# Kernel optimization log

Measured on AMD Instinct MI355X. Metric: run time of the kernel, lower is better.

## Reference

```python
import jax, jax.numpy as jnp
import numpy as np

T, H, E, I, IS = 1024, 2048, 64, 512, 1024
TOP_K = 8
CAP = 256


def setup_inputs() -> dict:
    key = jax.random.key(0)
    ks = jax.random.split(key, 9)
    s = 0.02
    return {
        "hidden_states": jax.random.normal(ks[0], (T, H), jnp.float32),
        "gate_w": jax.random.normal(ks[1], (E, H), jnp.float32) * s,
        "w1": jax.random.normal(ks[2], (E, H, I), jnp.float32) * s,
        "w3": jax.random.normal(ks[3], (E, H, I), jnp.float32) * s,
        "w2": jax.random.normal(ks[4], (E, I, H), jnp.float32) * s,
        "ws1": jax.random.normal(ks[5], (H, IS), jnp.float32) * s,
        "ws3": jax.random.normal(ks[6], (H, IS), jnp.float32) * s,
        "ws2": jax.random.normal(ks[7], (IS, H), jnp.float32) * s,
        "wsg": jax.random.normal(ks[8], (H, 1), jnp.float32) * s,
    }


def reference(hidden_states, gate_w, w1, w3, w2, ws1, ws3, ws2, wsg):
    x = hidden_states  # [T, H]
    n_tok = x.shape[0]

    # ---- router (Renormalize: top-k over logits, softmax over selected) ----
    logits = x @ gate_w.T                                  # [T, E]
    top_vals, top_idx = jax.lax.top_k(logits, TOP_K)       # [T, k]
    route_w = jax.nn.softmax(top_vals, axis=-1)            # renormalized weights

    # ---- dispatch: flatten (token, slot) assignments, rank within expert ----
    e = top_idx.reshape(-1)                                # [T*k] expert ids
    t = jnp.repeat(jnp.arange(n_tok), TOP_K)               # [T*k] token ids
    w_flat = route_w.reshape(-1)
    order = jnp.argsort(e, stable=True)
    counts = jax.ops.segment_sum(jnp.ones_like(e), e, num_segments=E)
    starts = jnp.cumsum(counts) - counts                   # exclusive cumsum
    pos_sorted = jnp.arange(e.shape[0]) - starts[e[order]]
    pos = jnp.zeros_like(e).at[order].set(pos_sorted)      # rank within expert
    valid = pos < CAP
    slot = jnp.where(valid, e * CAP + pos, E * CAP)        # overflow -> dump slot

    buf = jnp.zeros((E * CAP + 1, x.shape[1]), x.dtype).at[slot].set(x[t])
    xb = buf[:-1].reshape(E, CAP, x.shape[1])              # [E, C, H]

    # ---- grouped SwiGLU experts ----
    g = jax.nn.silu(jnp.einsum('ech,ehi->eci', xb, w1))
    u = jnp.einsum('ech,ehi->eci', xb, w3)
    yb = jnp.einsum('eci,eih->ech', g * u, w2).reshape(E * CAP, -1)

    # ---- combine ----
    contrib = yb[jnp.minimum(slot, E * CAP - 1)] * (w_flat * valid)[:, None]
    routed = jnp.zeros_like(x).at[t].add(contrib)

    # ---- shared expert with sigmoid gate ----
    shared = (jax.nn.silu(x @ ws1) * (x @ ws3)) @ ws2
    shared = jax.nn.sigmoid(x @ wsg) * shared

    return routed + shared
```

## Files before the change

### kernel.cpp

```cpp
#include <hip/hip_runtime.h>
#include <hip/hip_bf16.h>

#define NT    1024
#define HDIM  2048
#define NEXP  64
#define IDIM  512
#define ISDIM 1024
#define KTOP  8
#define ECAP  256

typedef float  f32x4 __attribute__((ext_vector_type(4)));
typedef __bf16 bf16x8 __attribute__((ext_vector_type(8)));
typedef unsigned short u16x8 __attribute__((ext_vector_type(8)));

static __device__ __forceinline__ unsigned short f2b(float f) {
  __hip_bfloat16 h = __float2bfloat16(f);
  return __builtin_bit_cast(unsigned short, h);
}
static __device__ __forceinline__ float b2f(unsigned short u) {
  return __bfloat162float(__builtin_bit_cast(__hip_bfloat16, u));
}
static __device__ __forceinline__ void sync_lds() {
  __builtin_amdgcn_s_waitcnt(0xc07f);
  __builtin_amdgcn_s_barrier();
}

__global__ __launch_bounds__(256) void k_router(
    const float* __restrict__ x, const float* __restrict__ gw,
    const float* __restrict__ wsg,
    int* __restrict__ counts, int* __restrict__ tok_list,
    int* __restrict__ slot_map, float* __restrict__ wgt_map,
    float* __restrict__ gate_sig)
{
  __shared__ float xs[HDIM];
  __shared__ float lg[NEXP];
  __shared__ float selv[KTOP];
  __shared__ int   sele[KTOP];
  const int t = blockIdx.x, tid = threadIdx.x;
  const float* xr = x + (size_t)t * HDIM;
  for (int i = tid; i < HDIM / 4; i += 256)
    ((f32x4*)xs)[i] = ((const f32x4*)xr)[i];
  __syncthreads();
  const int wave = tid >> 6, lane = tid & 63;
  for (int ei = 0; ei < 16; ++ei) {
    const int e = wave * 16 + ei;
    const float* g = gw + (size_t)e * HDIM;
    float s = 0.f;
    for (int j = lane; j < HDIM; j += 64) s += xs[j] * g[j];
    for (int off = 32; off; off >>= 1) s += __shfl_xor(s, off, 64);
    if (lane == 0) lg[e] = s;
  }
  if (wave == 1) {
    float s = 0.f;
    for (int j = lane; j < HDIM; j += 64) s += xs[j] * wsg[j];
    for (int off = 32; off; off >>= 1) s += __shfl_xor(s, off, 64);
    if (lane == 0) gate_sig[t] = 1.f / (1.f + __expf(-s));
  }
  __syncthreads();
  if (wave == 0) {
    float v = lg[lane];
    for (int k = 0; k < KTOP; ++k) {
      float m = v;
      for (int off = 32; off; off >>= 1) m = fmaxf(m, __shfl_xor(m, off, 64));
      unsigned long long msk = __ballot(v == m);
      int src = __ffsll(msk) - 1;
      if (lane == src) v = -3.4e38f;
      if (lane == 0) { selv[k] = m; sele[k] = src; }
    }
  }
  __syncthreads();
  if (tid < KTOP) {
    const int k = tid;
    const float mx = selv[0];
    float sum = 0.f;
    for (int i = 0; i < KTOP; ++i) sum += __expf(selv[i] - mx);
    const float w = __expf(selv[k] - mx) / sum;
    const int e = sele[k];
    const int pos = atomicAdd(&counts[e], 1);
    int slot = -1;
    if (pos < ECAP) { slot = e * ECAP + pos; tok_list[slot] = t; }
    slot_map[t * KTOP + k] = slot;
    wgt_map[t * KTOP + k] = w;
  }
}

__global__ __launch_bounds__(512, 2) void k_gemm1(
    const float* __restrict__ x,
    const float* __restrict__ w1, const float* __restrict__ w3,
    const float* __restrict__ ws1, const float* __restrict__ ws3,
    const int* __restrict__ counts, const int* __restrict__ tok_list,
    unsigned short* __restrict__ hbuf, unsigned short* __restrict__ hsbuf)
{
  __shared__ unsigned short lds[32768];
  const int g = blockIdx.y, ntile = blockIdx.x, tid = threadIdx.x;
  const bool is_exp = (g < NEXP);
  int me, ldb, m0s = 0;
  const float *b1p, *b3p;
  const int n0 = ntile * 128;
  if (is_exp) {
    if (ntile >= IDIM / 128) return;
    me = counts[g]; me = me < ECAP ? me : ECAP;
    if (me == 0) return;
    ldb = IDIM;
    b1p = w1 + (size_t)g * HDIM * IDIM + n0;
    b3p = w3 + (size_t)g * HDIM * IDIM + n0;
  } else {
    me = 256; ldb = ISDIM;
    m0s = (g - NEXP) * 256;
    b1p = ws1 + n0;
    b3p = ws3 + n0;
  }
  const int ar = tid >> 1, kh = (tid & 1) * 16;
  bool avalid;
  const float* arow;
  if (is_exp) {
    avalid = (ar < me);
    const int tok = avalid ? tok_list[g * ECAP + ar] : 0;
    arow = x + (size_t)tok * HDIM + kh;
  } else {
    avalid = true;
    arow = x + (size_t)(m0s + ar) * HDIM + kh;
  }
  const int ag0 = kh >> 3;
  const int aoff0 = ar * 32 + (((ag0 + 0) ^ (ar & 3)) << 3);
  const int aoff1 = ar * 32 + (((ag0 + 1) ^ (ar & 3)) << 3);
  const int bkr = tid >> 4, bc8 = (tid & 15) * 8;
  const float* b1t = b1p + (size_t)bkr * ldb + bc8;
  const float* b3t = b3p + (size_t)bkr * ldb + bc8;
  int boff[8];
#pragma unroll
  for (int i = 0; i < 8; ++i) {
    const int n = bc8 + i;
    boff[i] = n * 32 + (((bkr >> 3) ^ (n & 3)) << 3) + (bkr & 7);
  }
  const int lane = tid & 63, quad = lane >> 4, l15 = lane & 15;
  const int wv = tid >> 6, wm = wv >> 1, wn = wv & 1;
  const bool wactive = (wm * 64 < me);
  int aro[4], bo[4];
#pragma unroll
  for (int i = 0; i < 4; ++i) {
    const int rr = wm * 64 + i * 16 + l15;
    aro[i] = rr * 32 + ((quad ^ (rr & 3)) << 3);
    const int nn = wn * 64 + i * 16 + l15;
    bo[i] = nn * 32 + ((quad ^ (nn & 3)) << 3);
  }
  f32x4 acc1[4][4], acc3[4][4];
#pragma unroll
  for (int i = 0; i < 4; ++i)
#pragma unroll
    for (int j = 0; j < 4; ++j) {
      acc1[i][j] = f32x4{0.f, 0.f, 0.f, 0.f};
      acc3[i][j] = f32x4{0.f, 0.f, 0.f, 0.f};
    }
  f32x4 arg[4], b1r[2], b3r[2];
  const int KT = HDIM / 32;
  if (avalid) {
    arg[0] = ((const f32x4*)arow)[0]; arg[1] = ((const f32x4*)arow)[1];
    arg[2] = ((const f32x4*)arow)[2]; arg[3] = ((const f32x4*)arow)[3];
  }
  b1r[0] = ((const f32x4*)b1t)[0]; b1r[1] = ((const f32x4*)b1t)[1];
  b3r[0] = ((const f32x4*)b3t)[0]; b3r[1] = ((const f32x4*)b3t)[1];

  for (int kt = 0; kt < KT; ++kt) {
    unsigned short* L = lds + (kt & 1) * 16384;
    if (avalid) {
      u16x8 p0, p1;
#pragma unroll
      for (int i = 0; i < 4; ++i) {
        p0[i] = f2b(arg[0][i]); p0[4 + i] = f2b(arg[1][i]);
        p1[i] = f2b(arg[2][i]); p1[4 + i] = f2b(arg[3][i]);
      }
      *(u16x8*)&L[aoff0] = p0;
      *(u16x8*)&L[aoff1] = p1;
    }
    {
      unsigned short* B1 = L + 8192;
      unsigned short* B3 = L + 12288;
#pragma unroll
      for (int i = 0; i < 4; ++i) { B1[boff[i]] = f2b(b1r[0][i]); B1[boff[4 + i]] = f2b(b1r[1][i]); }
#pragma unroll
      for (int i = 0; i < 4; ++i) { B3[boff[i]] = f2b(b3r[0][i]); B3[boff[4 + i]] = f2b(b3r[1][i]); }
    }
    if (kt + 1 < KT) {
      const float* ap = arow + (kt + 1) * 32;
      if (avalid) {
        arg[0] = ((const f32x4*)ap)[0]; arg[1] = ((const f32x4*)ap)[1];
        arg[2] = ((const f32x4*)ap)[2]; arg[3] = ((const f32x4*)ap)[3];
      }
      const float* bp1 = b1t + (size_t)(kt + 1) * 32 * ldb;
      b1r[0] = ((const f32x4*)bp1)[0]; b1r[1] = ((const f32x4*)bp1)[1];
      const float* bp3 = b3t + (size_t)(kt + 1) * 32 * ldb;
      b3r[0] = ((const f32x4*)bp3)[0]; b3r[1] = ((const f32x4*)bp3)[1];
    }
    sync_lds();
    if (wactive) {
      bf16x8 af[4], bf1[4], bf3[4];
#pragma unroll
      for (int i = 0; i < 4; ++i)
        af[i] = __builtin_bit_cast(bf16x8, *(const u16x8*)&L[aro[i]]);
#pragma unroll
      for (int j = 0; j < 4; ++j) {
        bf1[j] = __builtin_bit_cast(bf16x8, *(const u16x8*)&L[8192 + bo[j]]);
        bf3[j] = __builtin_bit_cast(bf16x8, *(const u16x8*)&L[12288 + bo[j]]);
      }
#pragma unroll
      for (int i = 0; i < 4; ++i)
#pragma unroll
        for (int j = 0; j < 4; ++j) {
          acc1[i][j] = __builtin_amdgcn_mfma_f32_16x16x32_bf16(af[i], bf1[j], acc1[i][j], 0, 0, 0);
          acc3[i][j] = __builtin_amdgcn_mfma_f32_16x16x32_bf16(af[i], bf3[j], acc3[i][j], 0, 0, 0);
        }
    }
  }
  if (wactive) {
#pragma unroll
    for (int i = 0; i < 4; ++i) {
#pragma unroll
      for (int q = 0; q < 4; ++q) {
        const int rr = wm * 64 + i * 16 + quad * 4 + q;
        if (is_exp && rr >= me) continue;
        unsigned short* orow = is_exp
            ? hbuf + ((size_t)g * ECAP + rr) * IDIM
            : hsbuf + (size_t)(m0s + rr) * ISDIM;
#pragma unroll
        for (int j = 0; j < 4; ++j) {
          const int col = n0 + wn * 64 + j * 16 + l15;
          const float gg = acc1[i][j][q];
          const float uu = acc3[i][j][q];
          const float sv = (gg / (1.f + __expf(-gg))) * uu;
          orow[col] = f2b(sv);
        }
      }
    }
  }
}

__global__ __launch_bounds__(512, 2) void k_gemm2(
    const unsigned short* __restrict__ hbuf, const unsigned short* __restrict__ hsbuf,
    const float* __restrict__ w2, const float* __restrict__ ws2,
    const int* __restrict__ counts, const float* __restrict__ gate_sig,
    unsigned short* __restrict__ yb, float* __restrict__ out)
{
  __shared__ unsigned short lds[24576];
  const int g = blockIdx.y, ntile = blockIdx.x, tid = threadIdx.x;
  const bool is_exp = (g < NEXP);
  int me, K, m0s = 0;
  const unsigned short* abase;
  const float* bbase;
  const int n0 = ntile * 128;
  if (is_exp) {
    me = counts[g]; me = me < ECAP ? me : ECAP;
    if (me == 0) return;
    K = IDIM;
    abase = hbuf + (size_t)g * ECAP * IDIM;
    bbase = w2 + (size_t)g * IDIM * HDIM + n0;
  } else {
    me = 256; K = ISDIM;
    m0s = (g - NEXP) * 256;
    abase = hsbuf + (size_t)m0s * ISDIM;
    bbase = ws2 + n0;
  }
  const int ar = tid >> 1, kh = (tid & 1) * 16;
  const bool avalid = (ar < me);
  const unsigned short* arow = abase + (size_t)ar * K + kh;
  const int ag0 = kh >> 3;
  const int aoff0 = ar * 32 + (((ag0 + 0) ^ (ar & 3)) << 3);
  const int aoff1 = ar * 32 + (((ag0 + 1) ^ (ar & 3)) << 3);
  const int bkr = tid >> 4, bc8 = (tid & 15) * 8;
  const float* bt = bbase + (size_t)bkr * HDIM + bc8;
  int boff[8];
#pragma unroll
  for (int i = 0; i < 8; ++i) {
    const int n = bc8 + i;
    boff[i] = n * 32 + (((bkr >> 3) ^ (n & 3)) << 3) + (bkr & 7);
  }
  const int lane = tid & 63, quad = lane >> 4, l15 = lane & 15;
  const int wv = tid >> 6, wm = wv >> 1, wn = wv & 1;
  const bool wactive = (wm * 64 < me);
  int aro[4], bo[4];
#pragma unroll
  for (int i = 0; i < 4; ++i) {
    const int rr = wm * 64 + i * 16 + l15;
    aro[i] = rr * 32 + ((quad ^ (rr & 3)) << 3);
    const int nn = wn * 64 + i * 16 + l15;
    bo[i] = nn * 32 + ((quad ^ (nn & 3)) << 3);
  }
  f32x4 acc[4][4];
#pragma unroll
  for (int i = 0; i < 4; ++i)
#pragma unroll
    for (int j = 0; j < 4; ++j) acc[i][j] = f32x4{0.f, 0.f, 0.f, 0.f};
  u16x8 a0r, a1r;
  f32x4 br[2];
  const int KT = K / 32;
  if (avalid) { a0r = ((const u16x8*)arow)[0]; a1r = ((const u16x8*)arow)[1]; }
  br[0] = ((const f32x4*)bt)[0]; br[1] = ((const f32x4*)bt)[1];

  for (int kt = 0; kt < KT; ++kt) {
    unsigned short* L = lds + (kt & 1) * 12288;
    if (avalid) { *(u16x8*)&L[aoff0] = a0r; *(u16x8*)&L[aoff1] = a1r; }
    {
      unsigned short* B = L + 8192;
#pragma unroll
      for (int i = 0; i < 4; ++i) { B[boff[i]] = f2b(br[0][i]); B[boff[4 + i]] = f2b(br[1][i]); }
    }
    if (kt + 1 < KT) {
      const unsigned short* ap = arow + (kt + 1) * 32;
      if (avalid) { a0r = ((const u16x8*)ap)[0]; a1r = ((const u16x8*)ap)[1]; }
      const float* bp = bt + (size_t)(kt + 1) * 32 * HDIM;
      br[0] = ((const f32x4*)bp)[0]; br[1] = ((const f32x4*)bp)[1];
    }
    sync_lds();
    if (wactive) {
      bf16x8 af[4], bfr[4];
#pragma unroll
      for (int i = 0; i < 4; ++i)
        af[i] = __builtin_bit_cast(bf16x8, *(const u16x8*)&L[aro[i]]);
#pragma unroll
      for (int j = 0; j < 4; ++j)
        bfr[j] = __builtin_bit_cast(bf16x8, *(const u16x8*)&L[8192 + bo[j]]);
#pragma unroll
      for (int i = 0; i < 4; ++i)
#pragma unroll
        for (int j = 0; j < 4; ++j)
          acc[i][j] = __builtin_amdgcn_mfma_f32_16x16x32_bf16(af[i], bfr[j], acc[i][j], 0, 0, 0);
    }
  }
  if (wactive) {
#pragma unroll
    for (int i = 0; i < 4; ++i) {
#pragma unroll
      for (int q = 0; q < 4; ++q) {
        const int rr = wm * 64 + i * 16 + quad * 4 + q;
        if (is_exp) {
          if (rr >= me) continue;
          unsigned short* orow = yb + ((size_t)g * ECAP + rr) * HDIM;
#pragma unroll
          for (int j = 0; j < 4; ++j) {
            const int col = n0 + wn * 64 + j * 16 + l15;
            orow[col] = f2b(acc[i][j][q]);
          }
        } else {
          const float gt = gate_sig[m0s + rr];
          float* orow = out + (size_t)(m0s + rr) * HDIM;
#pragma unroll
          for (int j = 0; j < 4; ++j) {
            const int col = n0 + wn * 64 + j * 16 + l15;
            orow[col] = gt * acc[i][j][q];
          }
        }
      }
    }
  }
}

__global__ __launch_bounds__(256) void k_combine(
    const unsigned short* __restrict__ yb,
    const int* __restrict__ slot_map, const float* __restrict__ wgt_map,
    float* __restrict__ out)
{
  __shared__ int ss[KTOP];
  __shared__ float ww[KTOP];
  const int t = blockIdx.x, tid = threadIdx.x;
  if (tid < KTOP) { ss[tid] = slot_map[t * KTOP + tid]; ww[tid] = wgt_map[t * KTOP + tid]; }
  __syncthreads();
  const int c = tid * 8;
  float* op = out + (size_t)t * HDIM + c;
  f32x4 o0 = ((const f32x4*)op)[0];
  f32x4 o1 = ((const f32x4*)op)[1];
  for (int k = 0; k < KTOP; ++k) {
    const int s = ss[k];
    if (s < 0) continue;
    const float w = ww[k];
    const u16x8 y = *(const u16x8*)(yb + (size_t)s * HDIM + c);
#pragma unroll
    for (int i = 0; i < 4; ++i) {
      o0[i] += w * b2f(y[i]);
      o1[i] += w * b2f(y[4 + i]);
    }
  }
  ((f32x4*)op)[0] = o0;
  ((f32x4*)op)[1] = o1;
}

extern "C" void kernel_launch(void* const* d_in, const int* in_sizes, int n_in,
                              void* d_out, int out_size, void* d_ws, size_t ws_size,
                              hipStream_t stream) {
  (void)in_sizes; (void)n_in; (void)out_size; (void)ws_size;
  const float* x   = (const float*)d_in[0];
  const float* gw  = (const float*)d_in[1];
  const float* w1  = (const float*)d_in[2];
  const float* w3  = (const float*)d_in[3];
  const float* w2  = (const float*)d_in[4];
  const float* ws1 = (const float*)d_in[5];
  const float* ws3 = (const float*)d_in[6];
  const float* ws2 = (const float*)d_in[7];
  const float* wsg = (const float*)d_in[8];
  float* out = (float*)d_out;
  char* ws = (char*)d_ws;
  int*   counts   = (int*)ws;
  int*   tok_list = (int*)(ws + 256);
  int*   slot_map = (int*)(ws + 256 + (64 << 10));
  float* wgt_map  = (float*)(ws + 256 + (96 << 10));
  float* gate_sig = (float*)(ws + 256 + (128 << 10));
  unsigned short* hbuf  = (unsigned short*)(ws + (1 << 20));
  unsigned short* hsbuf = (unsigned short*)(ws + (17 << 20));
  unsigned short* yb    = (unsigned short*)(ws + (19 << 20));

  hipMemsetAsync(counts, 0, 256, stream);
  k_router<<<dim3(NT), dim3(256), 0, stream>>>(x, gw, wsg, counts, tok_list,
                                               slot_map, wgt_map, gate_sig);
  k_gemm1<<<dim3(8, NEXP + 4), dim3(512), 0, stream>>>(x, w1, w3, ws1, ws3,
                                                       counts, tok_list, hbuf, hsbuf);
  k_gemm2<<<dim3(16, NEXP + 4), dim3(512), 0, stream>>>(hbuf, hsbuf, w2, ws2,
                                                        counts, gate_sig, yb, out);
  k_combine<<<dim3(NT), dim3(256), 0, stream>>>(yb, slot_map, wgt_map, out);
}
```

Before: 1.250 ms.

## Flatten GEMM grids with XCD-aware block remap and vectorized B-tile LDS stores

Both grouped GEMM kernels now launch a flat 1D grid with no idle blocks and remap block IDs so consecutive logical tiles land on the same XCD (the remap assumes 8 chiplets), aiming for better L2 reuse of weights and expert inputs. The B-operand staging changes from row-vector loads with eight scalar LDS stores to column-wise scalar global loads (coalesced across threads) packed into one 16-byte LDS store per matrix. The LDS swizzle gains an extra XOR term to reduce bank conflicts. The trade-off is eight strided scalar global loads per thread per k-step instead of two vector loads.

New measurement: 1.099 ms. -12.0%, faster.

```diff
diff --git a/kernel.cpp b/kernel.cpp
--- a/kernel.cpp
+++ b/kernel.cpp
@@ -12,6 +12,8 @@
 typedef float  f32x4 __attribute__((ext_vector_type(4)));
 typedef __bf16 bf16x8 __attribute__((ext_vector_type(8)));
 typedef unsigned short u16x8 __attribute__((ext_vector_type(8)));
+
+#define SWZ(r, q) ((((q) ^ ((r) & 3) ^ (((r) >> 2) & 3)) & 3) << 3)
 
 static __device__ __forceinline__ unsigned short f2b(float f) {
   __hip_bfloat16 h = __float2bfloat16(f);
@@ -92,25 +94,33 @@
     unsigned short* __restrict__ hbuf, unsigned short* __restrict__ hsbuf)
 {
   __shared__ unsigned short lds[32768];
-  const int g = blockIdx.y, ntile = blockIdx.x, tid = threadIdx.x;
-  const bool is_exp = (g < NEXP);
-  int me, ldb, m0s = 0;
+  const int cpx = gridDim.x >> 3;
+  const int b0 = blockIdx.x;
+  const int bid = (b0 & 7) * cpx + (b0 >> 3);
+  const int tid = threadIdx.x;
+  bool is_exp;
+  int g, ntile, me, ldb, m0s = 0;
   const float *b1p, *b3p;
-  const int n0 = ntile * 128;
-  if (is_exp) {
-    if (ntile >= IDIM / 128) return;
+  if (bid < NEXP * 4) {
+    is_exp = true; g = bid >> 2; ntile = bid & 3;
     me = counts[g]; me = me < ECAP ? me : ECAP;
     if (me == 0) return;
     ldb = IDIM;
+  } else {
+    is_exp = false;
+    const int s = bid - NEXP * 4;
+    g = s >> 3; ntile = s & 7;
+    me = 256; ldb = ISDIM; m0s = g * 256;
+  }
+  const int n0 = ntile * 128;
+  if (is_exp) {
     b1p = w1 + (size_t)g * HDIM * IDIM + n0;
     b3p = w3 + (size_t)g * HDIM * IDIM + n0;
   } else {
-    me = 256; ldb = ISDIM;
-    m0s = (g - NEXP) * 256;
     b1p = ws1 + n0;
     b3p = ws3 + n0;
   }
-  const int ar = tid >> 1, kh = (tid & 1) * 16;
+  const int ar = tid & 255, sel = tid >> 8, kh = sel * 16;
   bool avalid;
   const float* arow;
   if (is_exp) {
@@ -121,18 +131,12 @@
     avalid = true;
     arow = x + (size_t)(m0s + ar) * HDIM + kh;
   }
-  const int ag0 = kh >> 3;
-  const int aoff0 = ar * 32 + (((ag0 + 0) ^ (ar & 3)) << 3);
-  const int aoff1 = ar * 32 + (((ag0 + 1) ^ (ar & 3)) << 3);
-  const int bkr = tid >> 4, bc8 = (tid & 15) * 8;
-  const float* b1t = b1p + (size_t)bkr * ldb + bc8;
-  const float* b3t = b3p + (size_t)bkr * ldb + bc8;
-  int boff[8];
-#pragma unroll
-  for (int i = 0; i < 8; ++i) {
-    const int n = bc8 + i;
-    boff[i] = n * 32 + (((bkr >> 3) ^ (n & 3)) << 3) + (bkr & 7);
-  }
+  const int aoff0 = ar * 32 + SWZ(ar, sel * 2);
+  const int aoff1 = ar * 32 + SWZ(ar, sel * 2 + 1);
+  const int bn = tid & 127, bg = tid >> 7;
+  const float* b1c = b1p + (size_t)(bg * 8) * ldb + bn;
+  const float* b3c = b3p + (size_t)(bg * 8) * ldb + bn;
+  const int boffB = bn * 32 + SWZ(bn, bg);
   const int lane = tid & 63, quad = lane >> 4, l15 = lane & 15;
   const int wv = tid >> 6, wm = wv >> 1, wn = wv & 1;
   const bool wactive = (wm * 64 < me);
@@ -140,9 +144,9 @@
 #pragma unroll
   for (int i = 0; i < 4; ++i) {
     const int rr = wm * 64 + i * 16 + l15;
-    aro[i] = rr * 32 + ((quad ^ (rr & 3)) << 3);
+    aro[i] = rr * 32 + SWZ(rr, quad);
     const int nn = wn * 64 + i * 16 + l15;
-    bo[i] = nn * 32 + ((quad ^ (nn & 3)) << 3);
+    bo[i] = nn * 32 + SWZ(nn, quad);
   }
   f32x4 acc1[4][4], acc3[4][4];
 #pragma unroll
@@ -152,14 +156,18 @@
       acc1[i][j] = f32x4{0.f, 0.f, 0.f, 0.f};
       acc3[i][j] = f32x4{0.f, 0.f, 0.f, 0.f};
     }
-  f32x4 arg[4], b1r[2], b3r[2];
+  f32x4 arg[4];
+  float b1v[8], b3v[8];
   const int KT = HDIM / 32;
   if (avalid) {
     arg[0] = ((const f32x4*)arow)[0]; arg[1] = ((const f32x4*)arow)[1];
     arg[2] = ((const f32x4*)arow)[2]; arg[3] = ((const f32x4*)arow)[3];
   }
-  b1r[0] = ((const f32x4*)b1t)[0]; b1r[1] = ((const f32x4*)b1t)[1];
-  b3r[0] = ((const f32x4*)b3t)[0]; b3r[1] = ((const f32x4*)b3t)[1];
+#pragma unroll
+  for (int j = 0; j < 8; ++j) {
+    b1v[j] = b1c[(size_t)j * ldb];
+    b3v[j] = b3c[(size_t)j * ldb];
+  }
 
   for (int kt = 0; kt < KT; ++kt) {
     unsigned short* L = lds + (kt & 1) * 16384;
@@ -174,12 +182,11 @@
       *(u16x8*)&L[aoff1] = p1;
     }
     {
-      unsigned short* B1 = L + 8192;
-      unsigned short* B3 = L + 12288;
-#pragma unroll
-      for (int i = 0; i < 4; ++i) { B1[boff[i]] = f2b(b1r[0][i]); B1[boff[4 + i]] = f2b(b1r[1][i]); }
-#pragma unroll
-      for (int i = 0; i < 4; ++i) { B3[boff[i]] = f2b(b3r[0][i]); B3[boff[4 + i]] = f2b(b3r[1][i]); }
+      u16x8 pb1, pb3;
+#pragma unroll
+      for (int j = 0; j < 8; ++j) { pb1[j] = f2b(b1v[j]); pb3[j] = f2b(b3v[j]); }
+      *(u16x8*)&L[8192 + boffB] = pb1;
+      *(u16x8*)&L[12288 + boffB] = pb3;
     }
     if (kt + 1 < KT) {
       const float* ap = arow + (kt + 1) * 32;
@@ -187,10 +194,13 @@
         arg[0] = ((const f32x4*)ap)[0]; arg[1] = ((const f32x4*)ap)[1];
         arg[2] = ((const f32x4*)ap)[2]; arg[3] = ((const f32x4*)ap)[3];
       }
-      const float* bp1 = b1t + (size_t)(kt + 1) * 32 * ldb;
-      b1r[0] = ((const f32x4*)bp1)[0]; b1r[1] = ((const f32x4*)bp1)[1];
-      const float* bp3 = b3t + (size_t)(kt + 1) * 32 * ldb;
-      b3r[0] = ((const f32x4*)bp3)[0]; b3r[1] = ((const f32x4*)bp3)[1];
+      const float* p1 = b1c + (size_t)(kt + 1) * 32 * ldb;
+      const float* p3 = b3c + (size_t)(kt + 1) * 32 * ldb;
+#pragma unroll
+      for (int j = 0; j < 8; ++j) {
+        b1v[j] = p1[(size_t)j * ldb];
+        b3v[j] = p3[(size_t)j * ldb];
+      }
     }
     sync_lds();
     if (wactive) {
@@ -242,38 +252,37 @@
     unsigned short* __restrict__ yb, float* __restrict__ out)
 {
   __shared__ unsigned short lds[24576];
-  const int g = blockIdx.y, ntile = blockIdx.x, tid = threadIdx.x;
-  const bool is_exp = (g < NEXP);
-  int me, K, m0s = 0;
+  const int cpx = gridDim.x >> 3;
+  const int b0 = blockIdx.x;
+  const int bid = (b0 & 7) * cpx + (b0 >> 3);
+  const int tid = threadIdx.x;
+  bool is_exp;
+  int g, ntile, me, K, m0s = 0;
   const unsigned short* abase;
   const float* bbase;
-  const int n0 = ntile * 128;
-  if (is_exp) {
+  if (bid < NEXP * 16) {
+    is_exp = true; g = bid >> 4; ntile = bid & 15;
     me = counts[g]; me = me < ECAP ? me : ECAP;
     if (me == 0) return;
     K = IDIM;
     abase = hbuf + (size_t)g * ECAP * IDIM;
-    bbase = w2 + (size_t)g * IDIM * HDIM + n0;
   } else {
-    me = 256; K = ISDIM;
-    m0s = (g - NEXP) * 256;
+    is_exp = false;
+    const int s = bid - NEXP * 16;
+    g = s >> 4; ntile = s & 15;
+    me = 256; K = ISDIM; m0s = g * 256;
     abase = hsbuf + (size_t)m0s * ISDIM;
-    bbase = ws2 + n0;
-  }
-  const int ar = tid >> 1, kh = (tid & 1) * 16;
+  }
+  const int n0 = ntile * 128;
+  bbase = is_exp ? (w2 + (size_t)g * IDIM * HDIM + n0) : (ws2 + n0);
+  const int ar = tid & 255, sel = tid >> 8, kh = sel * 16;
   const bool avalid = (ar < me);
   const unsigned short* arow = abase + (size_t)ar * K + kh;
-  const int ag0 = kh >> 3;
-  const int aoff0 = ar * 32 + (((ag0 + 0) ^ (ar & 3)) << 3);
-  const int aoff1 = ar * 32 + (((ag0 + 1) ^ (ar & 3)) << 3);
-  const int bkr = tid >> 4, bc8 = (tid & 15) * 8;
-  const float* bt = bbase + (size_t)bkr * HDIM + bc8;
-  int boff[8];
-#pragma unroll
-  for (int i = 0; i < 8; ++i) {
-    const int n = bc8 + i;
-    boff[i] = n * 32 + (((bkr >> 3) ^ (n & 3)) << 3) + (bkr & 7);
-  }
+  const int aoff0 = ar * 32 + SWZ(ar, sel * 2);
+  const int aoff1 = ar * 32 + SWZ(ar, sel * 2 + 1);
+  const int bn = tid & 127, bg = tid >> 7;
+  const float* bc = bbase + (size_t)(bg * 8) * HDIM + bn;
+  const int boffB = bn * 32 + SWZ(bn, bg);
   const int lane = tid & 63, quad = lane >> 4, l15 = lane & 15;
   const int wv = tid >> 6, wm = wv >> 1, wn = wv & 1;
   const bool wactive = (wm * 64 < me);
@@ -281,9 +290,9 @@
 #pragma unroll
   for (int i = 0; i < 4; ++i) {
     const int rr = wm * 64 + i * 16 + l15;
-    aro[i] = rr * 32 + ((quad ^ (rr & 3)) << 3);
+    aro[i] = rr * 32 + SWZ(rr, quad);
     const int nn = wn * 64 + i * 16 + l15;
-    bo[i] = nn * 32 + ((quad ^ (nn & 3)) << 3);
+    bo[i] = nn * 32 + SWZ(nn, quad);
   }
   f32x4 acc[4][4];
 #pragma unroll
@@ -291,24 +300,27 @@
 #pragma unroll
     for (int j = 0; j < 4; ++j) acc[i][j] = f32x4{0.f, 0.f, 0.f, 0.f};
   u16x8 a0r, a1r;
-  f32x4 br[2];
+  float bv[8];
   const int KT = K / 32;
   if (avalid) { a0r = ((const u16x8*)arow)[0]; a1r = ((const u16x8*)arow)[1]; }
-  br[0] = ((const f32x4*)bt)[0]; br[1] = ((const f32x4*)bt)[1];
+#pragma unroll
+  for (int j = 0; j < 8; ++j) bv[j] = bc[(size_t)j * HDIM];
 
   for (int kt = 0; kt < KT; ++kt) {
     unsigned short* L = lds + (kt & 1) * 12288;
     if (avalid) { *(u16x8*)&L[aoff0] = a0r; *(u16x8*)&L[aoff1] = a1r; }
     {
-      unsigned short* B = L + 8192;
-#pragma unroll
-      for (int i = 0; i < 4; ++i) { B[boff[i]] = f2b(br[0][i]); B[boff[4 + i]] = f2b(br[1][i]); }
+      u16x8 pb;
+#pragma unroll
+      for (int j = 0; j < 8; ++j) pb[j] = f2b(bv[j]);
+      *(u16x8*)&L[8192 + boffB] = pb;
     }
     if (kt + 1 < KT) {
       const unsigned short* ap = arow + (kt + 1) * 32;
       if (avalid) { a0r = ((const u16x8*)ap)[0]; a1r = ((const u16x8*)ap)[1]; }
-      const float* bp = bt + (size_t)(kt + 1) * 32 * HDIM;
-      br[0] = ((const f32x4*)bp)[0]; br[1] = ((const f32x4*)bp)[1];
+      const float* p = bc + (size_t)(kt + 1) * 32 * HDIM;
+#pragma unroll
+      for (int j = 0; j < 8; ++j) bv[j] = p[(size_t)j * HDIM];
     }
     sync_lds();
     if (wactive) {
@@ -410,9 +422,9 @@
   hipMemsetAsync(counts, 0, 256, stream);
   k_router<<<dim3(NT), dim3(256), 0, stream>>>(x, gw, wsg, counts, tok_list,
                                                slot_map, wgt_map, gate_sig);
-  k_gemm1<<<dim3(8, NEXP + 4), dim3(512), 0, stream>>>(x, w1, w3, ws1, ws3,
-                                                       counts, tok_list, hbuf, hsbuf);
-  k_gemm2<<<dim3(16, NEXP + 4), dim3(512), 0, stream>>>(hbuf, hsbuf, w2, ws2,
-                                                        counts, gate_sig, yb, out);
+  k_gemm1<<<dim3(NEXP * 4 + 32), dim3(512), 0, stream>>>(x, w1, w3, ws1, ws3,
+                                                         counts, tok_list, hbuf, hsbuf);
+  k_gemm2<<<dim3(NEXP * 16 + 64), dim3(512), 0, stream>>>(hbuf, hsbuf, w2, ws2,
+                                                          counts, gate_sig, yb, out);
   k_combine<<<dim3(NT), dim3(256), 0, stream>>>(yb, slot_map, wgt_map, out);
 }
```
